# Kernel tuning notes

Measured on AMD Instinct MI355X. Metric: run time of the kernel, lower is better.

Reference implementation:

```python
import jax, jax.numpy as jnp
import numpy as np

B, DIM, H_IN, H_OUT = 256, 16, 32, 32
IN_F, OUT_F = DIM * H_IN, DIM * H_OUT  # 512, 512


def _masks():
    rb = jnp.arange(OUT_F) // H_OUT  # row block id
    cb = jnp.arange(IN_F) // H_IN    # col block id
    mask_d = (rb[:, None] == cb[None, :]).astype(jnp.float32)  # block diagonal
    mask_o = (rb[:, None] > cb[None, :]).astype(jnp.float32)   # strictly lower block triangular
    return mask_d, mask_o


def setup_inputs() -> dict:
    key = jax.random.key(0)
    k1, k2, k3, k4, k5 = jax.random.split(key, 5)
    return {
        "inputs": jax.random.normal(k1, (B, IN_F), dtype=jnp.float32),
        "hyper_w": jax.random.normal(k2, (B, OUT_F, IN_F), dtype=jnp.float32),
        "hyper_b": jax.random.normal(k3, (B, OUT_F), dtype=jnp.float32),
        "log_grad_cumul": jax.random.normal(k4, (B, DIM, H_IN, 1), dtype=jnp.float32),
        "scale_factor": jax.random.uniform(k5, (1,), dtype=jnp.float32),
    }


def reference(inputs, hyper_w, hyper_b, log_grad_cumul, scale_factor):
    mask_d, mask_o = _masks()
    # per-sample weight build: exp on diagonal blocks, identity on lower blocks
    w = jnp.exp(hyper_w) * mask_d + hyper_w * mask_o  # [B, OUT, IN]
    # scaled Frobenius norm per sample
    w_F2 = jnp.sum(w * w, axis=(-2, -1), keepdims=True)  # [B,1,1]
    w_normed = jnp.exp(scale_factor) * w / jnp.sqrt(w_F2)
    # diagonal-block entries of hyper_w -> [B, DIM, H_OUT, H_IN]
    hw4 = hyper_w.reshape(B, DIM, H_OUT, DIM, H_IN)
    diag = jnp.moveaxis(jnp.diagonal(hw4, axis1=1, axis2=3), -1, 1)
    log_grad_dh = scale_factor + diag - 0.5 * jnp.log(w_F2)[..., None]
    # batched matvec + bias
    outputs = jnp.einsum('boi,bi->bo', w_normed, inputs) + hyper_b
    # logsumexp jacobian accumulation
    lg = log_grad_dh[..., None, :] + jnp.swapaxes(log_grad_cumul, -2, -1)[:, :, None, :, :]
    out_log_det = jax.scipy.special.logsumexp(lg, axis=-1)  # [B, DIM, H_OUT, 1]
    return outputs, out_log_det
```

## Files before the change

### kernel.cpp

```cpp
#include <hip/hip_runtime.h>
#include <math.h>


#define OUT_OFF 131072

typedef float f4 __attribute__((ext_vector_type(4)));

template<int RBA>
__device__ __forceinline__ void mw_body(
    const float* __restrict__ hw,
    const f4* __restrict__ xs,
    const f4* __restrict__ ls,
    float* __restrict__ sf,
    int b, int t,
    float* __restrict__ out,
    float* __restrict__ f2_partial)
{
    constexpr int RBB = 15 - RBA;
    const int r   = t >> 3;
    const int sub = t & 7;

    const f4* __restrict__ rowA = (const f4*)(hw + ((size_t)(b * 512 + RBA * 32 + r)) * 512);
    const f4* __restrict__ rowB = (const f4*)(hw + ((size_t)(b * 512 + RBB * 32 + r)) * 512);

    float accA = 0.f, f2A = 0.f, accB = 0.f, f2B = 0.f;

    #pragma unroll
    for (int j = 0; j < RBA; ++j) {
        f4 va = __builtin_nontemporal_load(rowA + j * 8 + sub);
        f4 vb = __builtin_nontemporal_load(rowB + j * 8 + sub);
        f4 xv = xs[j * 8 + sub];
        accA += va.x * xv.x + va.y * xv.y + va.z * xv.z + va.w * xv.w;
        f2A  += va.x * va.x + va.y * va.y + va.z * va.z + va.w * va.w;
        accB += vb.x * xv.x + vb.y * xv.y + vb.z * xv.z + vb.w * xv.w;
        f2B  += vb.x * vb.x + vb.y * vb.y + vb.z * vb.z + vb.w * vb.w;
    }
    #pragma unroll
    for (int j = RBA; j < RBB; ++j) {
        f4 vb = __builtin_nontemporal_load(rowB + j * 8 + sub);
        f4 xv = xs[j * 8 + sub];
        accB += vb.x * xv.x + vb.y * xv.y + vb.z * xv.z + vb.w * xv.w;
        f2B  += vb.x * vb.x + vb.y * vb.y + vb.z * vb.z + vb.w * vb.w;
    }

    float mA, sA, mB, sB;
    {
        f4 va = __builtin_nontemporal_load(rowA + RBA * 8 + sub);
        f4 vb = __builtin_nontemporal_load(rowB + RBB * 8 + sub);
        f4 xa = xs[RBA * 8 + sub];
        f4 xb = xs[RBB * 8 + sub];
        f4 la = ls[sub];
        f4 lb = ls[8 + sub];
        float e0 = expf(va.x), e1 = expf(va.y), e2 = expf(va.z), e3 = expf(va.w);
        accA += e0 * xa.x + e1 * xa.y + e2 * xa.z + e3 * xa.w;
        f2A  += e0 * e0 + e1 * e1 + e2 * e2 + e3 * e3;
        float a0 = va.x + la.x, a1 = va.y + la.y, a2 = va.z + la.z, a3 = va.w + la.w;
        mA = fmaxf(fmaxf(a0, a1), fmaxf(a2, a3));
        sA = expf(a0 - mA) + expf(a1 - mA) + expf(a2 - mA) + expf(a3 - mA);
        float g0 = expf(vb.x), g1 = expf(vb.y), g2 = expf(vb.z), g3 = expf(vb.w);
        accB += g0 * xb.x + g1 * xb.y + g2 * xb.z + g3 * xb.w;
        f2B  += g0 * g0 + g1 * g1 + g2 * g2 + g3 * g3;
        float b0 = vb.x + lb.x, b1 = vb.y + lb.y, b2 = vb.z + lb.z, b3 = vb.w + lb.w;
        mB = fmaxf(fmaxf(b0, b1), fmaxf(b2, b3));
        sB = expf(b0 - mB) + expf(b1 - mB) + expf(b2 - mB) + expf(b3 - mB);
    }

    #pragma unroll
    for (int d = 1; d < 8; d <<= 1) {
        accA += __shfl_xor(accA, d, 64);
        accB += __shfl_xor(accB, d, 64);
        float mo, so, mn;
        mo = __shfl_xor(mA, d, 64); so = __shfl_xor(sA, d, 64);
        mn = fmaxf(mA, mo); sA = sA * expf(mA - mn) + so * expf(mo - mn); mA = mn;
        mo = __shfl_xor(mB, d, 64); so = __shfl_xor(sB, d, 64);
        mn = fmaxf(mB, mo); sB = sB * expf(mB - mn) + so * expf(mo - mn); mB = mn;
    }
    if (sub == 0) {
        const int oA = RBA * 32 + r, oB = RBB * 32 + r;
        out[b * 512 + oA]           = accA;
        out[OUT_OFF + b * 512 + oA] = mA + logf(sA);
        out[b * 512 + oB]           = accB;
        out[OUT_OFF + b * 512 + oB] = mB + logf(sB);
    }

    float f2 = f2A + f2B;
    #pragma unroll
    for (int d = 1; d < 64; d <<= 1) f2 += __shfl_xor(f2, d, 64);
    if ((t & 63) == 0) sf[t >> 6] = f2;
    __syncthreads();
    if (t == 0) f2_partial[b * 8 + RBA] = sf[0] + sf[1] + sf[2] + sf[3];
}

__global__ __launch_bounds__(256) void mw_main(
    const float* __restrict__ hw,
    const float* __restrict__ x,
    const float* __restrict__ lgc,
    float* __restrict__ out,
    float* __restrict__ f2_partial)
{
    const int blk = blockIdx.x;
    const int b   = blk >> 3;
    const int pr  = blk & 7;
    const int rbA = pr, rbB = 15 - pr;
    const int t   = threadIdx.x;

    __shared__ f4 xs[128];
    __shared__ f4 ls[16];
    __shared__ float sf[4];
    if (t < 128) xs[t] = ((const f4*)(x + (size_t)b * 512))[t];
    if (t >= 128 && t < 136) ls[t - 128] = ((const f4*)(lgc + (size_t)b * 512 + rbA * 32))[t - 128];
    if (t >= 136 && t < 144) ls[t - 128] = ((const f4*)(lgc + (size_t)b * 512 + rbB * 32))[t - 136];
    __syncthreads();

    switch (pr) {
        case 0: mw_body<0>(hw, xs, ls, sf, b, t, out, f2_partial); break;
        case 1: mw_body<1>(hw, xs, ls, sf, b, t, out, f2_partial); break;
        case 2: mw_body<2>(hw, xs, ls, sf, b, t, out, f2_partial); break;
        case 3: mw_body<3>(hw, xs, ls, sf, b, t, out, f2_partial); break;
        case 4: mw_body<4>(hw, xs, ls, sf, b, t, out, f2_partial); break;
        case 5: mw_body<5>(hw, xs, ls, sf, b, t, out, f2_partial); break;
        case 6: mw_body<6>(hw, xs, ls, sf, b, t, out, f2_partial); break;
        case 7: mw_body<7>(hw, xs, ls, sf, b, t, out, f2_partial); break;
    }
}

__global__ __launch_bounds__(256) void mw_final(
    const float* __restrict__ f2_partial,
    const float* __restrict__ hb,
    const float* __restrict__ scale,
    float* __restrict__ out)
{
    const int b = blockIdx.x;
    const int t = threadIdx.x;

    float f2 = 0.0f;
    #pragma unroll
    for (int k = 0; k < 8; ++k) f2 += f2_partial[b * 8 + k];

    const float sc     = scale[0];
    const float coef   = expf(sc) / sqrtf(f2);
    const float logoff = sc - 0.5f * logf(f2);

    #pragma unroll
    for (int k = 0; k < 2; ++k) {
        const int o  = t + k * 256;
        const int io = b * 512 + o;
        out[io]           = coef * out[io] + hb[io];
        out[OUT_OFF + io] += logoff;
    }
}

extern "C" void kernel_launch(void* const* d_in, const int* in_sizes, int n_in,
                              void* d_out, int out_size, void* d_ws, size_t ws_size,
                              hipStream_t stream) {
    const float* x     = (const float*)d_in[0];
    const float* hw    = (const float*)d_in[1];
    const float* hb    = (const float*)d_in[2];
    const float* lgc   = (const float*)d_in[3];
    const float* scale = (const float*)d_in[4];
    float* out = (float*)d_out;
    float* f2p = (float*)d_ws;

    mw_main<<<dim3(256 * 8), dim3(256), 0, stream>>>(hw, x, lgc, out, f2p);
    mw_final<<<dim3(256), dim3(256), 0, stream>>>(f2p, hb, scale, out);
}
```

Before: 326.5 us.

## Fuse main and finalize kernels into one 1024-thread block per sample

Merges the two-kernel scheme (partial Frobenius sums written to workspace, then a finalize pass) into a single kernel with one 1024-thread block per batch sample. Each group of 256 threads handles two row-block pairs, keeps results in shared memory, reduces the norm in-block and writes scaled outputs with the bias directly. This removes the second launch and the global read-modify-write of the outputs. In exchange the grid shrinks from 2048 to 256 blocks, the inner loops have runtime bounds instead of templated full unrolling, and the nontemporal loads become plain loads, which may reduce memory-level parallelism on this bandwidth-bound stream.

```diff
diff --git a/kernel.cpp b/kernel.cpp
--- a/kernel.cpp
+++ b/kernel.cpp
@@ -6,147 +6,127 @@
 
 typedef float f4 __attribute__((ext_vector_type(4)));
 
-template<int RBA>
-__device__ __forceinline__ void mw_body(
-    const float* __restrict__ hw,
-    const f4* __restrict__ xs,
-    const f4* __restrict__ ls,
-    float* __restrict__ sf,
-    int b, int t,
-    float* __restrict__ out,
-    float* __restrict__ f2_partial)
-{
-    constexpr int RBB = 15 - RBA;
-    const int r   = t >> 3;
-    const int sub = t & 7;
-
-    const f4* __restrict__ rowA = (const f4*)(hw + ((size_t)(b * 512 + RBA * 32 + r)) * 512);
-    const f4* __restrict__ rowB = (const f4*)(hw + ((size_t)(b * 512 + RBB * 32 + r)) * 512);
-
-    float accA = 0.f, f2A = 0.f, accB = 0.f, f2B = 0.f;
-
-    #pragma unroll
-    for (int j = 0; j < RBA; ++j) {
-        f4 va = __builtin_nontemporal_load(rowA + j * 8 + sub);
-        f4 vb = __builtin_nontemporal_load(rowB + j * 8 + sub);
-        f4 xv = xs[j * 8 + sub];
-        accA += va.x * xv.x + va.y * xv.y + va.z * xv.z + va.w * xv.w;
-        f2A  += va.x * va.x + va.y * va.y + va.z * va.z + va.w * va.w;
-        accB += vb.x * xv.x + vb.y * xv.y + vb.z * xv.z + vb.w * xv.w;
-        f2B  += vb.x * vb.x + vb.y * vb.y + vb.z * vb.z + vb.w * vb.w;
-    }
-    #pragma unroll
-    for (int j = RBA; j < RBB; ++j) {
-        f4 vb = __builtin_nontemporal_load(rowB + j * 8 + sub);
-        f4 xv = xs[j * 8 + sub];
-        accB += vb.x * xv.x + vb.y * xv.y + vb.z * xv.z + vb.w * xv.w;
-        f2B  += vb.x * vb.x + vb.y * vb.y + vb.z * vb.z + vb.w * vb.w;
-    }
-
-    float mA, sA, mB, sB;
-    {
-        f4 va = __builtin_nontemporal_load(rowA + RBA * 8 + sub);
-        f4 vb = __builtin_nontemporal_load(rowB + RBB * 8 + sub);
-        f4 xa = xs[RBA * 8 + sub];
-        f4 xb = xs[RBB * 8 + sub];
-        f4 la = ls[sub];
-        f4 lb = ls[8 + sub];
-        float e0 = expf(va.x), e1 = expf(va.y), e2 = expf(va.z), e3 = expf(va.w);
-        accA += e0 * xa.x + e1 * xa.y + e2 * xa.z + e3 * xa.w;
-        f2A  += e0 * e0 + e1 * e1 + e2 * e2 + e3 * e3;
-        float a0 = va.x + la.x, a1 = va.y + la.y, a2 = va.z + la.z, a3 = va.w + la.w;
-        mA = fmaxf(fmaxf(a0, a1), fmaxf(a2, a3));
-        sA = expf(a0 - mA) + expf(a1 - mA) + expf(a2 - mA) + expf(a3 - mA);
-        float g0 = expf(vb.x), g1 = expf(vb.y), g2 = expf(vb.z), g3 = expf(vb.w);
-        accB += g0 * xb.x + g1 * xb.y + g2 * xb.z + g3 * xb.w;
-        f2B  += g0 * g0 + g1 * g1 + g2 * g2 + g3 * g3;
-        float b0 = vb.x + lb.x, b1 = vb.y + lb.y, b2 = vb.z + lb.z, b3 = vb.w + lb.w;
-        mB = fmaxf(fmaxf(b0, b1), fmaxf(b2, b3));
-        sB = expf(b0 - mB) + expf(b1 - mB) + expf(b2 - mB) + expf(b3 - mB);
-    }
-
-    #pragma unroll
-    for (int d = 1; d < 8; d <<= 1) {
-        accA += __shfl_xor(accA, d, 64);
-        accB += __shfl_xor(accB, d, 64);
-        float mo, so, mn;
-        mo = __shfl_xor(mA, d, 64); so = __shfl_xor(sA, d, 64);
-        mn = fmaxf(mA, mo); sA = sA * expf(mA - mn) + so * expf(mo - mn); mA = mn;
-        mo = __shfl_xor(mB, d, 64); so = __shfl_xor(sB, d, 64);
-        mn = fmaxf(mB, mo); sB = sB * expf(mB - mn) + so * expf(mo - mn); mB = mn;
-    }
-    if (sub == 0) {
-        const int oA = RBA * 32 + r, oB = RBB * 32 + r;
-        out[b * 512 + oA]           = accA;
-        out[OUT_OFF + b * 512 + oA] = mA + logf(sA);
-        out[b * 512 + oB]           = accB;
-        out[OUT_OFF + b * 512 + oB] = mB + logf(sB);
-    }
-
-    float f2 = f2A + f2B;
-    #pragma unroll
-    for (int d = 1; d < 64; d <<= 1) f2 += __shfl_xor(f2, d, 64);
-    if ((t & 63) == 0) sf[t >> 6] = f2;
-    __syncthreads();
-    if (t == 0) f2_partial[b * 8 + RBA] = sf[0] + sf[1] + sf[2] + sf[3];
-}
-
-__global__ __launch_bounds__(256) void mw_main(
+__global__ __launch_bounds__(1024) void mw_fused(
     const float* __restrict__ hw,
     const float* __restrict__ x,
     const float* __restrict__ lgc,
-    float* __restrict__ out,
-    float* __restrict__ f2_partial)
-{
-    const int blk = blockIdx.x;
-    const int b   = blk >> 3;
-    const int pr  = blk & 7;
-    const int rbA = pr, rbB = 15 - pr;
-    const int t   = threadIdx.x;
-
-    __shared__ f4 xs[128];
-    __shared__ f4 ls[16];
-    __shared__ float sf[4];
-    if (t < 128) xs[t] = ((const f4*)(x + (size_t)b * 512))[t];
-    if (t >= 128 && t < 136) ls[t - 128] = ((const f4*)(lgc + (size_t)b * 512 + rbA * 32))[t - 128];
-    if (t >= 136 && t < 144) ls[t - 128] = ((const f4*)(lgc + (size_t)b * 512 + rbB * 32))[t - 136];
-    __syncthreads();
-
-    switch (pr) {
-        case 0: mw_body<0>(hw, xs, ls, sf, b, t, out, f2_partial); break;
-        case 1: mw_body<1>(hw, xs, ls, sf, b, t, out, f2_partial); break;
-        case 2: mw_body<2>(hw, xs, ls, sf, b, t, out, f2_partial); break;
-        case 3: mw_body<3>(hw, xs, ls, sf, b, t, out, f2_partial); break;
-        case 4: mw_body<4>(hw, xs, ls, sf, b, t, out, f2_partial); break;
-        case 5: mw_body<5>(hw, xs, ls, sf, b, t, out, f2_partial); break;
-        case 6: mw_body<6>(hw, xs, ls, sf, b, t, out, f2_partial); break;
-        case 7: mw_body<7>(hw, xs, ls, sf, b, t, out, f2_partial); break;
-    }
-}
-
-__global__ __launch_bounds__(256) void mw_final(
-    const float* __restrict__ f2_partial,
     const float* __restrict__ hb,
     const float* __restrict__ scale,
     float* __restrict__ out)
 {
-    const int b = blockIdx.x;
-    const int t = threadIdx.x;
+    const int b   = blockIdx.x;
+    const int t   = threadIdx.x;
+    const int q   = t >> 8;
+    const int tt  = t & 255;
+    const int r   = tt >> 3;
+    const int sub = tt & 7;
 
-    float f2 = 0.0f;
-    #pragma unroll
-    for (int k = 0; k < 8; ++k) f2 += f2_partial[b * 8 + k];
+    __shared__ f4 xs[128];
+    __shared__ f4 ls[128];
+    __shared__ f4 outv[128];
+    __shared__ f4 lsev[128];
+    __shared__ float sfw[16];
 
-    const float sc     = scale[0];
-    const float coef   = expf(sc) / sqrtf(f2);
-    const float logoff = sc - 0.5f * logf(f2);
+    if (t < 128)      xs[t]       = ((const f4*)(x   + (size_t)b * 512))[t];
+    else if (t < 256) ls[t - 128] = ((const f4*)(lgc + (size_t)b * 512))[t - 128];
+    __syncthreads();
+
+    float f2 = 0.f;
 
     #pragma unroll
-    for (int k = 0; k < 2; ++k) {
-        const int o  = t + k * 256;
-        const int io = b * 512 + o;
-        out[io]           = coef * out[io] + hb[io];
-        out[OUT_OFF + io] += logoff;
+    for (int half = 0; half < 2; ++half) {
+        const int rbA = q + (half << 2);
+        const int rbB = 15 - rbA;
+        const int oA  = (rbA << 5) + r;
+        const int oB  = (rbB << 5) + r;
+        const f4* __restrict__ rowA = (const f4*)(hw + ((size_t)b * 512 + oA) * 512);
+        const f4* __restrict__ rowB = (const f4*)(hw + ((size_t)b * 512 + oB) * 512);
+
+        float accA = 0.f, accB = 0.f, fA = 0.f, fB = 0.f;
+
+        for (int j = 0; j < rbA; ++j) {
+            f4 va = rowA[j * 8 + sub];
+            f4 vb = rowB[j * 8 + sub];
+            f4 xv = xs[j * 8 + sub];
+            accA += va.x * xv.x + va.y * xv.y + va.z * xv.z + va.w * xv.w;
+            fA   += va.x * va.x + va.y * va.y + va.z * va.z + va.w * va.w;
+            accB += vb.x * xv.x + vb.y * xv.y + vb.z * xv.z + vb.w * xv.w;
+            fB   += vb.x * vb.x + vb.y * vb.y + vb.z * vb.z + vb.w * vb.w;
+        }
+        for (int j = rbA; j < rbB; ++j) {
+            f4 vb = rowB[j * 8 + sub];
+            f4 xv = xs[j * 8 + sub];
+            accB += vb.x * xv.x + vb.y * xv.y + vb.z * xv.z + vb.w * xv.w;
+            fB   += vb.x * vb.x + vb.y * vb.y + vb.z * vb.z + vb.w * vb.w;
+        }
+
+        float mA, sA, mB, sB;
+        {
+            f4 va = rowA[rbA * 8 + sub];
+            f4 vb = rowB[rbB * 8 + sub];
+            f4 xa = xs[rbA * 8 + sub];
+            f4 xb = xs[rbB * 8 + sub];
+            f4 la = ls[rbA * 8 + sub];
+            f4 lb = ls[rbB * 8 + sub];
+            float e0 = expf(va.x), e1 = expf(va.y), e2 = expf(va.z), e3 = expf(va.w);
+            accA += e0 * xa.x + e1 * xa.y + e2 * xa.z + e3 * xa.w;
+            fA   += e0 * e0 + e1 * e1 + e2 * e2 + e3 * e3;
+            float a0 = va.x + la.x, a1 = va.y + la.y, a2 = va.z + la.z, a3 = va.w + la.w;
+            mA = fmaxf(fmaxf(a0, a1), fmaxf(a2, a3));
+            sA = expf(a0 - mA) + expf(a1 - mA) + expf(a2 - mA) + expf(a3 - mA);
+            float g0 = expf(vb.x), g1 = expf(vb.y), g2 = expf(vb.z), g3 = expf(vb.w);
+            accB += g0 * xb.x + g1 * xb.y + g2 * xb.z + g3 * xb.w;
+            fB   += g0 * g0 + g1 * g1 + g2 * g2 + g3 * g3;
+            float b0 = vb.x + lb.x, b1 = vb.y + lb.y, b2 = vb.z + lb.z, b3 = vb.w + lb.w;
+            mB = fmaxf(fmaxf(b0, b1), fmaxf(b2, b3));
+            sB = expf(b0 - mB) + expf(b1 - mB) + expf(b2 - mB) + expf(b3 - mB);
+        }
+
+        #pragma unroll
+        for (int d = 1; d < 8; d <<= 1) {
+            accA += __shfl_xor(accA, d, 64);
+            accB += __shfl_xor(accB, d, 64);
+            float mo, so, mn;
+            mo = __shfl_xor(mA, d, 64); so = __shfl_xor(sA, d, 64);
+            mn = fmaxf(mA, mo); sA = sA * expf(mA - mn) + so * expf(mo - mn); mA = mn;
+            mo = __shfl_xor(mB, d, 64); so = __shfl_xor(sB, d, 64);
+            mn = fmaxf(mB, mo); sB = sB * expf(mB - mn) + so * expf(mo - mn); mB = mn;
+        }
+        if (sub == 0) {
+            ((float*)outv)[oA] = accA;
+            ((float*)lsev)[oA] = mA + logf(sA);
+            ((float*)outv)[oB] = accB;
+            ((float*)lsev)[oB] = mB + logf(sB);
+        }
+        f2 += fA + fB;
+    }
+
+    #pragma unroll
+    for (int d = 1; d < 64; d <<= 1) f2 += __shfl_xor(f2, d, 64);
+    if ((t & 63) == 0) sfw[t >> 6] = f2;
+    __syncthreads();
+
+    float f2t = 0.f;
+    #pragma unroll
+    for (int k = 0; k < 16; ++k) f2t += sfw[k];
+    const float sc     = scale[0];
+    const float coef   = expf(sc) / sqrtf(f2t);
+    const float logoff = sc - 0.5f * logf(f2t);
+
+    if (t < 128) {
+        f4 a = outv[t];
+        f4 h = ((const f4*)(hb + (size_t)b * 512))[t];
+        f4 o;
+        o.x = coef * a.x + h.x; o.y = coef * a.y + h.y;
+        o.z = coef * a.z + h.z; o.w = coef * a.w + h.w;
+        ((f4*)(out + (size_t)b * 512))[t] = o;
+    } else if (t < 256) {
+        const int i = t - 128;
+        f4 L = lsev[i];
+        f4 o;
+        o.x = L.x + logoff; o.y = L.y + logoff;
+        o.z = L.z + logoff; o.w = L.w + logoff;
+        ((f4*)(out + OUT_OFF + (size_t)b * 512))[i] = o;
     }
 }
 
@@ -159,8 +139,7 @@
     const float* lgc   = (const float*)d_in[3];
     const float* scale = (const float*)d_in[4];
     float* out = (float*)d_out;
-    float* f2p = (float*)d_ws;
+    (void)d_ws; (void)ws_size;
 
-    mw_main<<<dim3(256 * 8), dim3(256), 0, stream>>>(hw, x, lgc, out, f2p);
-    mw_final<<<dim3(256), dim3(256), 0, stream>>>(f2p, hb, scale, out);
+    mw_fused<<<dim3(256), dim3(1024), 0, stream>>>(hw, x, lgc, hb, scale, out);
 }
```

Result: slower. 336.8 us (+3.2%).
